# Kernel optimization log

Hardware: AMD Instinct MI355X
Metric: run time of the kernel (lower is better)

The kernel has to match this reference:

```python
import jax, jax.numpy as jnp
import numpy as np

G, N, F_IN, H, C = 128, 256, 128, 256, 10   # graphs, nodes/graph, in-feat, hidden, classes
NUM_NODES = G * N                            # 32768
E = NUM_NODES * 16                           # 524288 edges (avg degree 16)
K1, K2, K3 = 128, 64, 32                     # ceil(0.5*N) pooling chain per graph


def setup_inputs():
    key = jax.random.key(0)
    ks = jax.random.split(key, 16)
    def lin(k, fi, fo):
        return (jax.random.normal(k, (fi, fo), jnp.float32) / np.sqrt(fi).astype(np.float32))
    x = jax.random.normal(ks[0], (NUM_NODES, F_IN), jnp.float32)
    gid = jnp.repeat(jnp.arange(G), E // G)
    src = (gid * N + jax.random.randint(ks[1], (E,), 0, N)).astype(jnp.int32)
    dst = (gid * N + jax.random.randint(ks[2], (E,), 0, N)).astype(jnp.int32)
    edge_index = jnp.stack([src, dst])
    batch = jnp.repeat(jnp.arange(G), N).astype(jnp.int32)
    z32 = lambda *s: jnp.zeros(s, jnp.float32)
    return dict(
        x=x, edge_index=edge_index, batch=batch,
        conv1_W=lin(ks[3], F_IN, H), conv1_b=z32(H),
        conv2_W=lin(ks[4], H, H), conv2_b=z32(H),
        conv3_W=lin(ks[5], H, H), conv3_b=z32(H),
        pool1_rel_W=lin(ks[6], H, 1), pool1_rel_b=z32(1), pool1_root_W=lin(ks[7], H, 1),
        pool2_rel_W=lin(ks[8], H, 1), pool2_rel_b=z32(1), pool2_root_W=lin(ks[9], H, 1),
        fc1_W=lin(ks[10], 3 * H, H), fc1_b=z32(H),
        fc2_W=lin(ks[11], H, H // 2), fc2_b=z32(H // 2),
        fc3_W=lin(ks[12], H // 2, C), fc3_b=z32(C))


def _gcn(x, W, b, src, dst, emask, nmask):
    # PyG GCNConv: out = D^{-1/2}(A+I)D^{-1/2} (x W) + b, masked nodes/edges excluded.
    h = x @ W
    ew = emask.astype(x.dtype)
    deg = jax.ops.segment_sum(ew, dst, num_segments=NUM_NODES) + nmask  # +1 self-loop for active nodes
    dis = jnp.where(deg > 0, jax.lax.rsqrt(jnp.maximum(deg, 1e-12)), 0.0)
    norm = dis[src] * dis[dst] * ew
    out = jax.ops.segment_sum(h[src] * norm[:, None], dst, num_segments=NUM_NODES)
    out = out + h * (dis * dis * nmask)[:, None]  # self-loop message
    return out + b


def _sag_pool(x, src, dst, emask, nmask, k, w_rel, b_rel, w_root):
    # score = GraphConv(x): lin_root(x) + lin_rel(sum_j x_j); then top-k per graph, x *= tanh(score)
    ew = emask.astype(x.dtype)
    agg = jax.ops.segment_sum(x[src] * ew[:, None], dst, num_segments=NUM_NODES)
    score = (agg @ w_rel + b_rel + x @ w_root)[:, 0]
    score = jnp.where(nmask > 0, score, -jnp.inf)
    _, idx = jax.lax.top_k(score.reshape(G, N), k)           # [G, k] within-graph indices
    newmask = jnp.zeros((G, N), x.dtype).at[jnp.arange(G)[:, None], idx].set(1.0).reshape(-1)
    x = x * jnp.tanh(score)[:, None] * newmask[:, None]
    emask = emask & (newmask[src] > 0) & (newmask[dst] > 0)
    return x, emask, newmask


def _readout(x, nmask):
    xg = x.reshape(G, N, -1)
    m = nmask.reshape(G, N, 1)
    s = (xg * m).sum(axis=1)                                  # add-pool
    mean = s / m.sum(axis=1)                                  # mean-pool
    mx = jnp.max(jnp.where(m > 0, xg, -jnp.inf), axis=1)      # max-pool
    return jnp.concatenate([mean, mx, s], axis=-1)            # [G, 3H]


def reference(x, edge_index, batch, conv1_W, conv1_b, conv2_W, conv2_b, conv3_W, conv3_b,
              pool1_rel_W, pool1_rel_b, pool1_root_W, pool2_rel_W, pool2_rel_b, pool2_root_W,
              fc1_W, fc1_b, fc2_W, fc2_b, fc3_W, fc3_b):
    src, dst = edge_index[0], edge_index[1]
    nmask = jnp.ones((NUM_NODES,), x.dtype)
    emask = jnp.ones((E,), bool)
    h = jax.nn.relu(_gcn(x, conv1_W, conv1_b, src, dst, emask, nmask))
    h, emask, nmask = _sag_pool(h, src, dst, emask, nmask, K1, pool1_rel_W, pool1_rel_b, pool1_root_W)
    x1 = _readout(h, nmask)
    h = jax.nn.relu(_gcn(h, conv2_W, conv2_b, src, dst, emask, nmask))
    h, emask, nmask = _sag_pool(h, src, dst, emask, nmask, K2, pool2_rel_W, pool2_rel_b, pool2_root_W)
    x2 = _readout(h, nmask)
    h = jax.nn.relu(_gcn(h, conv3_W, conv3_b, src, dst, emask, nmask))
    # NB: original source reuses self.pool2 for the third pooling stage
    h, emask, nmask = _sag_pool(h, src, dst, emask, nmask, K3, pool2_rel_W, pool2_rel_b, pool2_root_W)
    x3 = _readout(h, nmask)
    z = x1 + x2 + x3
    z = jax.nn.relu(z @ fc1_W + fc1_b)
    z = jax.nn.relu(z @ fc2_W + fc2_b)          # dropout is identity in eval mode
    return jax.nn.log_softmax(z @ fc3_W + fc3_b, axis=-1)
```

## Files before the change

kernel.cpp:

```cpp
#include <hip/hip_runtime.h>
#include <math.h>

#define NG 128
#define NPG 256
#define NN 32768
#define HDIM 256
#define FIN 128

__global__ __launch_bounds__(256) void k_csr(const int* __restrict__ esrc,
                                             const int* __restrict__ edst, int EPG,
                                             int* __restrict__ rowptr, int* __restrict__ csr) {
    __shared__ int cnt[NPG];
    __shared__ int pref[NPG];
    __shared__ int cur[NPG];
    int g = blockIdx.x, tid = threadIdx.x;
    cnt[tid] = 0;
    __syncthreads();
    int base = g * EPG;
    for (int e = base + tid; e < base + EPG; e += 256)
        atomicAdd(&cnt[edst[e] & (NPG - 1)], 1);
    __syncthreads();
    int v = cnt[tid];
    pref[tid] = v;
    __syncthreads();
    for (int off = 1; off < NPG; off <<= 1) {
        int t = (tid >= off) ? pref[tid - off] : 0;
        __syncthreads();
        pref[tid] += t;
        __syncthreads();
    }
    int excl = pref[tid] - v;
    rowptr[g * NPG + tid] = base + excl;
    cur[tid] = base + excl;
    if (g == 0 && tid == 0) rowptr[NN] = NG * EPG;
    __syncthreads();
    for (int e = base + tid; e < base + EPG; e += 256) {
        int d = edst[e] & (NPG - 1);
        int p = atomicAdd(&cur[d], 1);
        csr[p] = esrc[e];
    }
}

__global__ __launch_bounds__(256) void k_sortw(const int* __restrict__ rowptr,
                                               int* __restrict__ csr,
                                               float* __restrict__ wedge) {
    int wid = (blockIdx.x * blockDim.x + threadIdx.x) >> 6;
    int lane = threadIdx.x & 63;
    if (wid >= NN) return;
    int e0 = rowptr[wid];
    int d = rowptr[wid + 1] - e0;
    if (d == 0) return;
    float ddst = rsqrtf((float)(1 + d));
    if (d <= 64) {
        int key = (lane < d) ? csr[e0 + lane] : 0x7fffffff;
        int rank = 0;
        for (int j = 0; j < d; j++) {
            int kj = __shfl(key, j);
            rank += (kj < key || (kj == key && j < lane)) ? 1 : 0;
        }
        if (lane < d) {
            csr[e0 + rank] = key;
            int sdeg = rowptr[key + 1] - rowptr[key];
            wedge[e0 + rank] = rsqrtf((float)(1 + sdeg)) * ddst;
        }
    } else if (lane == 0) {
        for (int a = e0 + 1; a < e0 + d; a++) {
            int key = csr[a];
            int b = a - 1;
            while (b >= e0 && csr[b] > key) { csr[b + 1] = csr[b]; b--; }
            csr[b + 1] = key;
        }
        for (int a = e0; a < e0 + d; a++) {
            int s = csr[a];
            wedge[a] = rsqrtf((float)(1 + rowptr[s + 1] - rowptr[s])) * ddst;
        }
    }
}

#define BM 64
#define BN 64
#define BK 16
#define BMP 68
__global__ __launch_bounds__(256) void k_sgemm(const float* __restrict__ A,
                                               const float* __restrict__ B,
                                               float* __restrict__ C, int K,
                                               const int* __restrict__ list,
                                               const float* __restrict__ brelu,
                                               const float* __restrict__ wrel,
                                               const float* __restrict__ wroot,
                                               float* __restrict__ rrel4,
                                               float* __restrict__ rroot4) {
    const int N = HDIM;
    __shared__ float As[BK][BMP];
    __shared__ float Bs[BK][BN];
    int tid = threadIdx.x;
    int tx = tid & 15, ty = tid >> 4;
    int row0 = blockIdx.y * BM, col0 = blockIdx.x * BN;
    int lm = tid >> 2;
    int arow = list ? list[row0 + lm] : (row0 + lm);
    int crow[4];
#pragma unroll
    for (int i = 0; i < 4; i++) {
        int r = row0 + ty * 4 + i;
        crow[i] = list ? list[r] : r;
    }
    float acc[4][4] = {};
    for (int kb = 0; kb < K; kb += BK) {
        {
            int k = (tid & 3) * 4;
            float4 av = *reinterpret_cast<const float4*>(&A[(size_t)arow * K + kb + k]);
            As[k + 0][lm] = av.x; As[k + 1][lm] = av.y; As[k + 2][lm] = av.z; As[k + 3][lm] = av.w;
        }
        {
            int l = tid * 4;
            int k = l >> 6, c = l & 63;
            *reinterpret_cast<float4*>(&Bs[k][c]) =
                *reinterpret_cast<const float4*>(&B[(size_t)(kb + k) * N + col0 + c]);
        }
        __syncthreads();
#pragma unroll
        for (int k = 0; k < BK; k++) {
            float4 a = *reinterpret_cast<float4*>(&As[k][ty * 4]);
            float4 b = *reinterpret_cast<float4*>(&Bs[k][tx * 4]);
            float av[4] = {a.x, a.y, a.z, a.w};
            float bv[4] = {b.x, b.y, b.z, b.w};
#pragma unroll
            for (int i = 0; i < 4; i++)
#pragma unroll
                for (int j = 0; j < 4; j++) acc[i][j] += av[i] * bv[j];
        }
        __syncthreads();
    }
    float4 bb = make_float4(0.f, 0.f, 0.f, 0.f);
    if (brelu) bb = *reinterpret_cast<const float4*>(&brelu[col0 + tx * 4]);
    float4 wr = make_float4(0.f, 0.f, 0.f, 0.f), wo = wr;
    if (wrel) {
        wr = *reinterpret_cast<const float4*>(&wrel[col0 + tx * 4]);
        wo = *reinterpret_cast<const float4*>(&wroot[col0 + tx * 4]);
    }
#pragma unroll
    for (int i = 0; i < 4; i++) {
        float4 v = make_float4(acc[i][0], acc[i][1], acc[i][2], acc[i][3]);
        if (brelu) {
            v.x = fmaxf(v.x + bb.x, 0.f);
            v.y = fmaxf(v.y + bb.y, 0.f);
            v.z = fmaxf(v.z + bb.z, 0.f);
            v.w = fmaxf(v.w + bb.w, 0.f);
        }
        *reinterpret_cast<float4*>(&C[(size_t)crow[i] * N + col0 + tx * 4]) = v;
        if (wrel) {
            float s1 = v.x * wr.x + v.y * wr.y + v.z * wr.z + v.w * wr.w;
            float s2 = v.x * wo.x + v.y * wo.y + v.z * wo.z + v.w * wo.w;
            for (int off = 8; off > 0; off >>= 1) {
                s1 += __shfl_down(s1, off, 16);
                s2 += __shfl_down(s2, off, 16);
            }
            if (tx == 0) {
                rrel4[(size_t)crow[i] * 4 + blockIdx.x] = s1;
                rroot4[(size_t)crow[i] * 4 + blockIdx.x] = s2;
            }
        }
    }
}

__device__ __forceinline__ int swz_block(int bid, int bpg) {
    int xcd = bid & 7, r = bid >> 3;
    int graph = xcd * (NG / 8) + r / bpg;
    int sub = r - (r / bpg) * bpg;
    return graph * bpg + sub;
}

__global__ __launch_bounds__(256) void k_aggx(const float* __restrict__ x,
                                              const int* __restrict__ rowptr,
                                              const int* __restrict__ csr,
                                              const float* __restrict__ wedge,
                                              float* __restrict__ xa) {
    int blk = swz_block(blockIdx.x, NPG / 8);
    int n = blk * 8 + (threadIdx.x >> 5);
    int lane = threadIdx.x & 31;
    const float4* xp = reinterpret_cast<const float4*>(x);
    int e0 = rowptr[n], e1 = rowptr[n + 1];
    float di = rsqrtf((float)(1 + e1 - e0));
    float4 h = xp[(size_t)n * (FIN / 4) + lane];
    float self = di * di;
    float ax = h.x * self, ay = h.y * self, az = h.z * self, aw = h.w * self;
    for (int e = e0; e < e1; e++) {
        int s = csr[e];
        float w = wedge[e];
        float4 hs = xp[(size_t)s * (FIN / 4) + lane];
        ax += hs.x * w; ay += hs.y * w; az += hs.z * w; aw += hs.w * w;
    }
    float4 o = make_float4(ax, ay, az, aw);
    reinterpret_cast<float4*>(xa)[(size_t)n * (FIN / 4) + lane] = o;
}

__global__ __launch_bounds__(256) void k_gcn_agg(const float* __restrict__ hW,
                                                 const float* __restrict__ dis,
                                                 const int* __restrict__ rowptr,
                                                 const int* __restrict__ csr,
                                                 const float* __restrict__ wedge,
                                                 const float* __restrict__ bias,
                                                 const int* __restrict__ list, int bpg,
                                                 const float* __restrict__ w_rel,
                                                 const float* __restrict__ w_root,
                                                 float* __restrict__ out,
                                                 float* __restrict__ r_rel,
                                                 float* __restrict__ r_root) {
    int blk = swz_block(blockIdx.x, bpg);
    int idx = blk * 4 + (threadIdx.x >> 6);
    int lane = threadIdx.x & 63;
    int wid = list[idx];
    float di = dis[wid];
    float4 h = *reinterpret_cast<const float4*>(&hW[(size_t)wid * HDIM + lane * 4]);
    float self = di * di;
    float ax = h.x * self, ay = h.y * self, az = h.z * self, aw = h.w * self;
    int e0 = rowptr[wid], e1 = rowptr[wid + 1];
    for (int e = e0; e < e1; e++) {
        float w = wedge[e];
        if (w > 0.f) {
            int s = csr[e];
            float4 hs = *reinterpret_cast<const float4*>(&hW[(size_t)s * HDIM + lane * 4]);
            ax += hs.x * w; ay += hs.y * w; az += hs.z * w; aw += hs.w * w;
        }
    }
    float4 b = *reinterpret_cast<const float4*>(&bias[lane * 4]);
    float4 o;
    o.x = fmaxf(ax + b.x, 0.f);
    o.y = fmaxf(ay + b.y, 0.f);
    o.z = fmaxf(az + b.z, 0.f);
    o.w = fmaxf(aw + b.w, 0.f);
    *reinterpret_cast<float4*>(&out[(size_t)wid * HDIM + lane * 4]) = o;
    float4 wr = *reinterpret_cast<const float4*>(&w_rel[lane * 4]);
    float4 wo = *reinterpret_cast<const float4*>(&w_root[lane * 4]);
    float s1 = o.x * wr.x + o.y * wr.y + o.z * wr.z + o.w * wr.w;
    float s2 = o.x * wo.x + o.y * wo.y + o.z * wo.z + o.w * wo.w;
    for (int off = 32; off > 0; off >>= 1) {
        s1 += __shfl_down(s1, off);
        s2 += __shfl_down(s2, off);
    }
    if (lane == 0) { r_rel[wid] = s1; r_root[wid] = s2; }
}

template<bool STAGE1, bool EMIT>
__global__ __launch_bounds__(256) void k_topkf(const float* __restrict__ dis,
                                               const int* __restrict__ rowptr,
                                               const int* __restrict__ csr,
                                               const float* __restrict__ r_rel,
                                               const float* __restrict__ r_root,
                                               const float* __restrict__ rrel4,
                                               const float* __restrict__ rroot4,
                                               const float* __restrict__ b_rel, int k,
                                               int* __restrict__ list,
                                               float* __restrict__ tansel,
                                               float* __restrict__ disN,
                                               float* __restrict__ wedgeN) {
    __shared__ float rrel[NPG];
    __shared__ float sc[NPG];
    __shared__ int pref[NPG];
    __shared__ int sels[NPG];
    __shared__ float disn[NPG];
    int g = blockIdx.x, tid = threadIdx.x;
    int n = g * NPG + tid;
    bool act = STAGE1 ? true : (dis[n] > 0.f);
    float rr, ro;
    if (STAGE1) {
        rr = ((rrel4[(size_t)n * 4 + 0] + rrel4[(size_t)n * 4 + 1]) +
              rrel4[(size_t)n * 4 + 2]) + rrel4[(size_t)n * 4 + 3];
        ro = ((rroot4[(size_t)n * 4 + 0] + rroot4[(size_t)n * 4 + 1]) +
              rroot4[(size_t)n * 4 + 2]) + rroot4[(size_t)n * 4 + 3];
    } else {
        rr = act ? r_rel[n] : 0.f;
        ro = act ? r_root[n] : 0.f;
    }
    rrel[tid] = act ? rr : 0.f;
    __syncthreads();
    int e0 = rowptr[n], e1 = rowptr[n + 1];
    float my;
    if (act) {
        float s = b_rel[0] + ro;
        for (int e = e0; e < e1; e++) s += rrel[csr[e] & (NPG - 1)];
        my = s;
    } else {
        my = -INFINITY;
    }
    sc[tid] = my;
    __syncthreads();
    int cnt = 0;
    for (int j = 0; j < NPG; j++) {
        float v = sc[j];
        cnt += (v > my || (v == my && j < tid)) ? 1 : 0;
    }
    int a = (cnt < k) ? 1 : 0;
    sels[tid] = a;
    pref[tid] = a;
    __syncthreads();
    for (int off = 1; off < NPG; off <<= 1) {
        int v = (tid >= off) ? pref[tid - off] : 0;
        __syncthreads();
        pref[tid] += v;
        __syncthreads();
    }
    if (a) {
        int rk = pref[tid] - 1;
        list[g * k + rk] = n;
        tansel[g * k + rk] = tanhf(my);
    }
    if (EMIT) {
        int c2 = 1;
        for (int e = e0; e < e1; e++) c2 += sels[csr[e] & (NPG - 1)];
        float dn = a ? rsqrtf((float)c2) : 0.f;
        disn[tid] = dn;
        disN[n] = dn;
        __syncthreads();
        if (a) {
            for (int e = e0; e < e1; e++) wedgeN[e] = disn[csr[e] & (NPG - 1)] * dn;
        }
    }
}

template<bool FIRST>
__global__ __launch_bounds__(256) void k_poolout2(float* __restrict__ h,
                                                  const float* __restrict__ tansel,
                                                  const int* __restrict__ list, int k,
                                                  float invk, float* __restrict__ z) {
    __shared__ float tv[128];
    __shared__ float red_s[4][64];
    __shared__ float red_m[4][64];
    int g = blockIdx.x >> 2, fc = blockIdx.x & 3;
    int tid = threadIdx.x;
    int x = tid & 63, y = tid >> 6;
    if (tid < k) tv[tid] = tansel[g * k + tid];
    __syncthreads();
    int f = fc * 64 + x;
    float s = 0.f, mx = -INFINITY;
    for (int idx = y; idx < k; idx += 4) {
        int node = list[g * k + idx];
        size_t p = (size_t)node * HDIM + f;
        float v = h[p] * tv[idx];
        h[p] = v;
        s += v;
        mx = fmaxf(mx, v);
    }
    red_s[y][x] = s;
    red_m[y][x] = mx;
    __syncthreads();
    if (y == 0) {
        s = red_s[0][x] + red_s[1][x] + red_s[2][x] + red_s[3][x];
        mx = fmaxf(fmaxf(red_m[0][x], red_m[1][x]), fmaxf(red_m[2][x], red_m[3][x]));
        if (FIRST) {
            z[g * 768 + f] = s * invk;
            z[g * 768 + 256 + f] = mx;
            z[g * 768 + 512 + f] = s;
        } else {
            z[g * 768 + f] += s * invk;
            z[g * 768 + 256 + f] += mx;
            z[g * 768 + 512 + f] += s;
        }
    }
}

__global__ __launch_bounds__(256) void k_fc1(const float* __restrict__ z,
                                             const float* __restrict__ W1,
                                             const float* __restrict__ b1,
                                             float* __restrict__ t1) {
    __shared__ float zb[768];
    __shared__ float red[4][64];
    int g = blockIdx.x >> 2, oc = blockIdx.x & 3;
    int tid = threadIdx.x;
    zb[tid] = z[g * 768 + tid];
    zb[tid + 256] = z[g * 768 + 256 + tid];
    zb[tid + 512] = z[g * 768 + 512 + tid];
    __syncthreads();
    int x = tid & 63, y = tid >> 6;
    int col = oc * 64 + x;
    float s = 0.f;
    for (int i = y * 192; i < (y + 1) * 192; i++) s += zb[i] * W1[(size_t)i * 256 + col];
    red[y][x] = s;
    __syncthreads();
    if (y == 0) {
        float t = red[0][x] + red[1][x] + red[2][x] + red[3][x] + b1[col];
        t1[g * 256 + col] = fmaxf(t, 0.f);
    }
}

__global__ __launch_bounds__(256) void k_fc2(const float* __restrict__ t1,
                                             const float* __restrict__ W2,
                                             const float* __restrict__ b2,
                                             float* __restrict__ t2) {
    __shared__ float t1s[256];
    __shared__ float red[4][64];
    int g = blockIdx.x >> 1, oc = blockIdx.x & 1;
    int tid = threadIdx.x;
    t1s[tid] = t1[g * 256 + tid];
    __syncthreads();
    int x = tid & 63, y = tid >> 6;
    int col = oc * 64 + x;
    float s = 0.f;
    for (int i = y * 64; i < (y + 1) * 64; i++) s += t1s[i] * W2[(size_t)i * 128 + col];
    red[y][x] = s;
    __syncthreads();
    if (y == 0) {
        float t = ((red[0][x] + red[1][x]) + red[2][x]) + red[3][x] + b2[col];
        t2[g * 128 + col] = fmaxf(t, 0.f);
    }
}

__global__ __launch_bounds__(256) void k_fc3(const float* __restrict__ t2,
                                             const float* __restrict__ W3,
                                             const float* __restrict__ b3,
                                             float* __restrict__ out) {
    __shared__ float t2s[128];
    __shared__ float t3[10];
    __shared__ float lse;
    int g = blockIdx.x, tid = threadIdx.x;
    if (tid < 128) t2s[tid] = t2[g * 128 + tid];
    __syncthreads();
    if (tid < 10) {
        float v = b3[tid];
        for (int i = 0; i < 128; i++) v += t2s[i] * W3[(size_t)i * 10 + tid];
        t3[tid] = v;
    }
    __syncthreads();
    if (tid == 0) {
        float m = t3[0];
        for (int c = 1; c < 10; c++) m = fmaxf(m, t3[c]);
        float se = 0.f;
        for (int c = 0; c < 10; c++) se += expf(t3[c] - m);
        lse = m + logf(se);
    }
    __syncthreads();
    if (tid < 10) out[g * 10 + tid] = t3[tid] - lse;
}

extern "C" void kernel_launch(void* const* d_in, const int* in_sizes, int n_in,
                              void* d_out, int out_size, void* d_ws, size_t ws_size,
                              hipStream_t stream) {
    const float* x        = (const float*)d_in[0];
    const int*   ei       = (const int*)d_in[1];
    const float* conv1_W  = (const float*)d_in[3];
    const float* conv1_b  = (const float*)d_in[4];
    const float* conv2_W  = (const float*)d_in[5];
    const float* conv2_b  = (const float*)d_in[6];
    const float* conv3_W  = (const float*)d_in[7];
    const float* conv3_b  = (const float*)d_in[8];
    const float* p1_relW  = (const float*)d_in[9];
    const float* p1_relb  = (const float*)d_in[10];
    const float* p1_rootW = (const float*)d_in[11];
    const float* p2_relW  = (const float*)d_in[12];
    const float* p2_relb  = (const float*)d_in[13];
    const float* p2_rootW = (const float*)d_in[14];
    const float* fc1_W    = (const float*)d_in[15];
    const float* fc1_b    = (const float*)d_in[16];
    const float* fc2_W    = (const float*)d_in[17];
    const float* fc2_b    = (const float*)d_in[18];
    const float* fc3_W    = (const float*)d_in[19];
    const float* fc3_b    = (const float*)d_in[20];
    float* out = (float*)d_out;

    const int E = in_sizes[1] / 2;
    const int EPG = E / NG;
    const int* e_src = ei;
    const int* e_dst = ei + E;

    char* base = (char*)d_ws;
    size_t off = 0;
    auto alloc = [&](size_t bytes) { size_t o = off; off = (off + bytes + 255) & ~(size_t)255; return o; };
    float* hW     = (float*)(base + alloc((size_t)NN * HDIM * 4));
    float* hcur   = (float*)(base + alloc((size_t)NN * HDIM * 4));
    float* dis    = (float*)(base + alloc(NN * 4));
    float* r_rel  = (float*)(base + alloc(NN * 4));
    float* r_root = (float*)(base + alloc(NN * 4));
    float* rrel4  = (float*)(base + alloc((size_t)NN * 4 * 4));
    float* rroot4 = (float*)(base + alloc((size_t)NN * 4 * 4));
    int*   rowptr = (int*)(base + alloc((NN + 1) * 4));
    int*   csr    = (int*)(base + alloc((size_t)E * 4));
    float* wedge  = (float*)(base + alloc((size_t)E * 4));
    float* z      = (float*)(base + alloc((size_t)NG * 768 * 4));
    float* t1buf  = (float*)(base + alloc((size_t)NG * 256 * 4));
    float* t2buf  = (float*)(base + alloc((size_t)NG * 128 * 4));
    int*   list1  = (int*)(base + alloc((size_t)NG * 128 * 4));
    int*   list2  = (int*)(base + alloc((size_t)NG * 64 * 4));
    int*   list3  = (int*)(base + alloc((size_t)NG * 32 * 4));
    float* tans1  = (float*)(base + alloc((size_t)NG * 128 * 4));
    float* tans2  = (float*)(base + alloc((size_t)NG * 64 * 4));
    float* tans3  = (float*)(base + alloc((size_t)NG * 32 * 4));

    k_csr<<<NG, 256, 0, stream>>>(e_src, e_dst, EPG, rowptr, csr);
    k_sortw<<<NN * 64 / 256, 256, 0, stream>>>(rowptr, csr, wedge);

    float* xa = hW;

    k_aggx<<<NN / 8, 256, 0, stream>>>(x, rowptr, csr, wedge, xa);
    {
        dim3 ggrid(HDIM / BN, NN / BM);
        k_sgemm<<<ggrid, 256, 0, stream>>>(xa, conv1_W, hcur, FIN, nullptr, conv1_b,
                                           p1_relW, p1_rootW, rrel4, rroot4);
    }
    k_topkf<true, true><<<NG, 256, 0, stream>>>(nullptr, rowptr, csr, nullptr, nullptr,
                                                rrel4, rroot4, p1_relb, 128,
                                                list1, tans1, dis, wedge);
    k_poolout2<true><<<NG * 4, 256, 0, stream>>>(hcur, tans1, list1, 128, 1.0f / 128.0f, z);

    {
        dim3 ggrid(HDIM / BN, (NG * 128) / BM);
        k_sgemm<<<ggrid, 256, 0, stream>>>(hcur, conv2_W, hW, HDIM, list1, nullptr,
                                           nullptr, nullptr, nullptr, nullptr);
    }
    k_gcn_agg<<<(NG * 128) / 4, 256, 0, stream>>>(hW, dis, rowptr, csr, wedge, conv2_b,
                                                  list1, 32, p2_relW, p2_rootW,
                                                  hcur, r_rel, r_root);
    k_topkf<false, true><<<NG, 256, 0, stream>>>(dis, rowptr, csr, r_rel, r_root,
                                                 nullptr, nullptr, p2_relb, 64,
                                                 list2, tans2, dis, wedge);
    k_poolout2<false><<<NG * 4, 256, 0, stream>>>(hcur, tans2, list2, 64, 1.0f / 64.0f, z);

    {
        dim3 ggrid(HDIM / BN, (NG * 64) / BM);
        k_sgemm<<<ggrid, 256, 0, stream>>>(hcur, conv3_W, hW, HDIM, list2, nullptr,
                                           nullptr, nullptr, nullptr, nullptr);
    }
    k_gcn_agg<<<(NG * 64) / 4, 256, 0, stream>>>(hW, dis, rowptr, csr, wedge, conv3_b,
                                                 list2, 16, p2_relW, p2_rootW,
                                                 hcur, r_rel, r_root);
    k_topkf<false, false><<<NG, 256, 0, stream>>>(dis, rowptr, csr, r_rel, r_root,
                                                  nullptr, nullptr, p2_relb, 32,
                                                  list3, tans3, nullptr, nullptr);
    k_poolout2<false><<<NG * 4, 256, 0, stream>>>(hcur, tans3, list3, 32, 1.0f / 32.0f, z);

    k_fc1<<<NG * 4, 256, 0, stream>>>(z, fc1_W, fc1_b, t1buf);
    k_fc2<<<NG * 2, 256, 0, stream>>>(t1buf, fc2_W, fc2_b, t2buf);
    k_fc3<<<NG, 256, 0, stream>>>(t2buf, fc3_W, fc3_b, out);
}
```

Before: 309.1 us.

## Fuse CSR sort with aggregation, top-k with pooling, and MLP layers; prefetch GEMM tiles

```diff
diff --git a/kernel.cpp b/kernel.cpp
--- a/kernel.cpp
+++ b/kernel.cpp
@@ -41,17 +41,27 @@
     }
 }
 
-__global__ __launch_bounds__(256) void k_sortw(const int* __restrict__ rowptr,
-                                               int* __restrict__ csr,
-                                               float* __restrict__ wedge) {
-    int wid = (blockIdx.x * blockDim.x + threadIdx.x) >> 6;
-    int lane = threadIdx.x & 63;
-    if (wid >= NN) return;
-    int e0 = rowptr[wid];
-    int d = rowptr[wid + 1] - e0;
-    if (d == 0) return;
+__device__ __forceinline__ int swz_block(int bid, int bpg) {
+    int xcd = bid & 7, r = bid >> 3;
+    int graph = xcd * (NG / 8) + r / bpg;
+    int sub = r - (r / bpg) * bpg;
+    return graph * bpg + sub;
+}
+
+__global__ __launch_bounds__(256) void k_sortagg(const float* __restrict__ x,
+                                                 const int* __restrict__ rowptr,
+                                                 int* __restrict__ csr,
+                                                 float* __restrict__ xa) {
+    __shared__ int skey[4][64];
+    __shared__ float swgt[4][64];
+    int blk = swz_block(blockIdx.x, NPG / 4);
+    int w = threadIdx.x >> 6, lane = threadIdx.x & 63;
+    int n = blk * 4 + w;
+    int e0 = rowptr[n];
+    int d = rowptr[n + 1] - e0;
     float ddst = rsqrtf((float)(1 + d));
-    if (d <= 64) {
+    bool big = d > 64;
+    if (!big) {
         int key = (lane < d) ? csr[e0 + lane] : 0x7fffffff;
         int rank = 0;
         for (int j = 0; j < d; j++) {
@@ -60,8 +70,8 @@
         }
         if (lane < d) {
             csr[e0 + rank] = key;
-            int sdeg = rowptr[key + 1] - rowptr[key];
-            wedge[e0 + rank] = rsqrtf((float)(1 + sdeg)) * ddst;
+            skey[w][rank] = key;
+            swgt[w][rank] = rsqrtf((float)(1 + rowptr[key + 1] - rowptr[key])) * ddst;
         }
     } else if (lane == 0) {
         for (int a = e0 + 1; a < e0 + d; a++) {
@@ -70,11 +80,30 @@
             while (b >= e0 && csr[b] > key) { csr[b + 1] = csr[b]; b--; }
             csr[b + 1] = key;
         }
-        for (int a = e0; a < e0 + d; a++) {
-            int s = csr[a];
-            wedge[a] = rsqrtf((float)(1 + rowptr[s + 1] - rowptr[s])) * ddst;
-        }
-    }
+    }
+    __syncthreads();
+    const float2* x2 = reinterpret_cast<const float2*>(x);
+    float di = ddst;
+    float2 h = x2[(size_t)n * (FIN / 2) + lane];
+    float self = di * di;
+    float ax = h.x * self, ay = h.y * self;
+    if (!big) {
+        for (int j = 0; j < d; j++) {
+            int s = skey[w][j];
+            float we = swgt[w][j];
+            float2 hs = x2[(size_t)s * (FIN / 2) + lane];
+            ax += hs.x * we; ay += hs.y * we;
+        }
+    } else {
+        for (int e = e0; e < e0 + d; e++) {
+            int s = csr[e];
+            float we = rsqrtf((float)(1 + rowptr[s + 1] - rowptr[s])) * ddst;
+            float2 hs = x2[(size_t)s * (FIN / 2) + lane];
+            ax += hs.x * we; ay += hs.y * we;
+        }
+    }
+    float2 o; o.x = ax; o.y = ay;
+    reinterpret_cast<float2*>(xa)[(size_t)n * (FIN / 2) + lane] = o;
 }
 
 #define BM 64
@@ -104,20 +133,20 @@
         int r = row0 + ty * 4 + i;
         crow[i] = list ? list[r] : r;
     }
+    int k4 = (tid & 3) * 4;
+    int kkB = tid >> 4, cB = (tid & 15) * 4;
+    float4 aP = *reinterpret_cast<const float4*>(&A[(size_t)arow * K + k4]);
+    float4 bP = *reinterpret_cast<const float4*>(&B[(size_t)kkB * N + col0 + cB]);
     float acc[4][4] = {};
     for (int kb = 0; kb < K; kb += BK) {
-        {
-            int k = (tid & 3) * 4;
-            float4 av = *reinterpret_cast<const float4*>(&A[(size_t)arow * K + kb + k]);
-            As[k + 0][lm] = av.x; As[k + 1][lm] = av.y; As[k + 2][lm] = av.z; As[k + 3][lm] = av.w;
-        }
-        {
-            int l = tid * 4;
-            int k = l >> 6, c = l & 63;
-            *reinterpret_cast<float4*>(&Bs[k][c]) =
-                *reinterpret_cast<const float4*>(&B[(size_t)(kb + k) * N + col0 + c]);
-        }
-        __syncthreads();
+        As[k4 + 0][lm] = aP.x; As[k4 + 1][lm] = aP.y;
+        As[k4 + 2][lm] = aP.z; As[k4 + 3][lm] = aP.w;
+        *reinterpret_cast<float4*>(&Bs[kkB][cB]) = bP;
+        __syncthreads();
+        if (kb + BK < K) {
+            aP = *reinterpret_cast<const float4*>(&A[(size_t)arow * K + kb + BK + k4]);
+            bP = *reinterpret_cast<const float4*>(&B[(size_t)(kb + BK + kkB) * N + col0 + cB]);
+        }
 #pragma unroll
         for (int k = 0; k < BK; k++) {
             float4 a = *reinterpret_cast<float4*>(&As[k][ty * 4]);
@@ -161,37 +190,6 @@
             }
         }
     }
-}
-
-__device__ __forceinline__ int swz_block(int bid, int bpg) {
-    int xcd = bid & 7, r = bid >> 3;
-    int graph = xcd * (NG / 8) + r / bpg;
-    int sub = r - (r / bpg) * bpg;
-    return graph * bpg + sub;
-}
-
-__global__ __launch_bounds__(256) void k_aggx(const float* __restrict__ x,
-                                              const int* __restrict__ rowptr,
-                                              const int* __restrict__ csr,
-                                              const float* __restrict__ wedge,
-                                              float* __restrict__ xa) {
-    int blk = swz_block(blockIdx.x, NPG / 8);
-    int n = blk * 8 + (threadIdx.x >> 5);
-    int lane = threadIdx.x & 31;
-    const float4* xp = reinterpret_cast<const float4*>(x);
-    int e0 = rowptr[n], e1 = rowptr[n + 1];
-    float di = rsqrtf((float)(1 + e1 - e0));
-    float4 h = xp[(size_t)n * (FIN / 4) + lane];
-    float self = di * di;
-    float ax = h.x * self, ay = h.y * self, az = h.z * self, aw = h.w * self;
-    for (int e = e0; e < e1; e++) {
-        int s = csr[e];
-        float w = wedge[e];
-        float4 hs = xp[(size_t)s * (FIN / 4) + lane];
-        ax += hs.x * w; ay += hs.y * w; az += hs.z * w; aw += hs.w * w;
-    }
-    float4 o = make_float4(ax, ay, az, aw);
-    reinterpret_cast<float4*>(xa)[(size_t)n * (FIN / 4) + lane] = o;
 }
 
 __global__ __launch_bounds__(256) void k_gcn_agg(const float* __restrict__ hW,
@@ -241,25 +239,31 @@
     if (lane == 0) { r_rel[wid] = s1; r_root[wid] = s2; }
 }
 
-template<bool STAGE1, bool EMIT>
-__global__ __launch_bounds__(256) void k_topkf(const float* __restrict__ dis,
-                                               const int* __restrict__ rowptr,
-                                               const int* __restrict__ csr,
-                                               const float* __restrict__ r_rel,
-                                               const float* __restrict__ r_root,
-                                               const float* __restrict__ rrel4,
-                                               const float* __restrict__ rroot4,
-                                               const float* __restrict__ b_rel, int k,
-                                               int* __restrict__ list,
-                                               float* __restrict__ tansel,
-                                               float* __restrict__ disN,
-                                               float* __restrict__ wedgeN) {
+template<bool STAGE1, bool EMIT, bool FIRST>
+__global__ __launch_bounds__(256) void k_topkpool(const float* __restrict__ dis,
+                                                  const int* __restrict__ rowptr,
+                                                  const int* __restrict__ csr,
+                                                  const float* __restrict__ r_rel,
+                                                  const float* __restrict__ r_root,
+                                                  const float* __restrict__ rrel4,
+                                                  const float* __restrict__ rroot4,
+                                                  const float* __restrict__ b_rel, int k,
+                                                  int* __restrict__ list,
+                                                  float* __restrict__ h,
+                                                  float* __restrict__ z, float invk,
+                                                  float* __restrict__ disN,
+                                                  float* __restrict__ wedgeN) {
     __shared__ float rrel[NPG];
     __shared__ float sc[NPG];
     __shared__ int pref[NPG];
     __shared__ int sels[NPG];
     __shared__ float disn[NPG];
-    int g = blockIdx.x, tid = threadIdx.x;
+    __shared__ int newl[128];
+    __shared__ float tvsel[128];
+    __shared__ float red_s[4][64];
+    __shared__ float red_m[4][64];
+    int g = blockIdx.x >> 2, fc = blockIdx.x & 3;
+    int tid = threadIdx.x;
     int n = g * NPG + tid;
     bool act = STAGE1 ? true : (dis[n] > 0.f);
     float rr, ro;
@@ -302,51 +306,39 @@
     }
     if (a) {
         int rk = pref[tid] - 1;
-        list[g * k + rk] = n;
-        tansel[g * k + rk] = tanhf(my);
+        newl[rk] = tid;
+        tvsel[rk] = tanhf(my);
+        if (fc == 0 && list) list[g * k + rk] = n;
     }
     if (EMIT) {
         int c2 = 1;
         for (int e = e0; e < e1; e++) c2 += sels[csr[e] & (NPG - 1)];
         float dn = a ? rsqrtf((float)c2) : 0.f;
         disn[tid] = dn;
-        disN[n] = dn;
-        __syncthreads();
-        if (a) {
+        if (fc == 0) disN[n] = dn;
+        __syncthreads();
+        if (a && fc == 0) {
             for (int e = e0; e < e1; e++) wedgeN[e] = disn[csr[e] & (NPG - 1)] * dn;
         }
     }
-}
-
-template<bool FIRST>
-__global__ __launch_bounds__(256) void k_poolout2(float* __restrict__ h,
-                                                  const float* __restrict__ tansel,
-                                                  const int* __restrict__ list, int k,
-                                                  float invk, float* __restrict__ z) {
-    __shared__ float tv[128];
-    __shared__ float red_s[4][64];
-    __shared__ float red_m[4][64];
-    int g = blockIdx.x >> 2, fc = blockIdx.x & 3;
-    int tid = threadIdx.x;
-    int x = tid & 63, y = tid >> 6;
-    if (tid < k) tv[tid] = tansel[g * k + tid];
-    __syncthreads();
-    int f = fc * 64 + x;
+    __syncthreads();
+    int xq = tid & 63, y = tid >> 6;
+    int f = fc * 64 + xq;
     float s = 0.f, mx = -INFINITY;
     for (int idx = y; idx < k; idx += 4) {
-        int node = list[g * k + idx];
+        int node = g * NPG + newl[idx];
         size_t p = (size_t)node * HDIM + f;
-        float v = h[p] * tv[idx];
+        float v = h[p] * tvsel[idx];
         h[p] = v;
         s += v;
         mx = fmaxf(mx, v);
     }
-    red_s[y][x] = s;
-    red_m[y][x] = mx;
+    red_s[y][xq] = s;
+    red_m[y][xq] = mx;
     __syncthreads();
     if (y == 0) {
-        s = red_s[0][x] + red_s[1][x] + red_s[2][x] + red_s[3][x];
-        mx = fmaxf(fmaxf(red_m[0][x], red_m[1][x]), fmaxf(red_m[2][x], red_m[3][x]));
+        s = red_s[0][xq] + red_s[1][xq] + red_s[2][xq] + red_s[3][xq];
+        mx = fmaxf(fmaxf(red_m[0][xq], red_m[1][xq]), fmaxf(red_m[2][xq], red_m[3][xq]));
         if (FIRST) {
             z[g * 768 + f] = s * invk;
             z[g * 768 + 256 + f] = mx;
@@ -359,65 +351,44 @@
     }
 }
 
-__global__ __launch_bounds__(256) void k_fc1(const float* __restrict__ z,
-                                             const float* __restrict__ W1,
-                                             const float* __restrict__ b1,
-                                             float* __restrict__ t1) {
+__global__ __launch_bounds__(256) void k_mlp(const float* __restrict__ z,
+                                             const float* __restrict__ W1, const float* __restrict__ b1,
+                                             const float* __restrict__ W2, const float* __restrict__ b2,
+                                             const float* __restrict__ W3, const float* __restrict__ b3,
+                                             float* __restrict__ out) {
     __shared__ float zb[768];
-    __shared__ float red[4][64];
-    int g = blockIdx.x >> 2, oc = blockIdx.x & 3;
-    int tid = threadIdx.x;
+    __shared__ float t1[256];
+    __shared__ float t2[128];
+    __shared__ float t3[10];
+    __shared__ float lse;
+    int g = blockIdx.x, tid = threadIdx.x;
     zb[tid] = z[g * 768 + tid];
     zb[tid + 256] = z[g * 768 + 256 + tid];
     zb[tid + 512] = z[g * 768 + 512 + tid];
     __syncthreads();
-    int x = tid & 63, y = tid >> 6;
-    int col = oc * 64 + x;
-    float s = 0.f;
-    for (int i = y * 192; i < (y + 1) * 192; i++) s += zb[i] * W1[(size_t)i * 256 + col];
-    red[y][x] = s;
-    __syncthreads();
-    if (y == 0) {
-        float t = red[0][x] + red[1][x] + red[2][x] + red[3][x] + b1[col];
-        t1[g * 256 + col] = fmaxf(t, 0.f);
-    }
-}
-
-__global__ __launch_bounds__(256) void k_fc2(const float* __restrict__ t1,
-                                             const float* __restrict__ W2,
-                                             const float* __restrict__ b2,
-                                             float* __restrict__ t2) {
-    __shared__ float t1s[256];
-    __shared__ float red[4][64];
-    int g = blockIdx.x >> 1, oc = blockIdx.x & 1;
-    int tid = threadIdx.x;
-    t1s[tid] = t1[g * 256 + tid];
-    __syncthreads();
-    int x = tid & 63, y = tid >> 6;
-    int col = oc * 64 + x;
-    float s = 0.f;
-    for (int i = y * 64; i < (y + 1) * 64; i++) s += t1s[i] * W2[(size_t)i * 128 + col];
-    red[y][x] = s;
-    __syncthreads();
-    if (y == 0) {
-        float t = ((red[0][x] + red[1][x]) + red[2][x]) + red[3][x] + b2[col];
-        t2[g * 128 + col] = fmaxf(t, 0.f);
-    }
-}
-
-__global__ __launch_bounds__(256) void k_fc3(const float* __restrict__ t2,
-                                             const float* __restrict__ W3,
-                                             const float* __restrict__ b3,
-                                             float* __restrict__ out) {
-    __shared__ float t2s[128];
-    __shared__ float t3[10];
-    __shared__ float lse;
-    int g = blockIdx.x, tid = threadIdx.x;
-    if (tid < 128) t2s[tid] = t2[g * 128 + tid];
+    {
+        int col = tid;
+        float r0 = 0.f, r1 = 0.f, r2 = 0.f, r3 = 0.f;
+        for (int i = 0;   i < 192; i++) r0 += zb[i] * W1[(size_t)i * 256 + col];
+        for (int i = 192; i < 384; i++) r1 += zb[i] * W1[(size_t)i * 256 + col];
+        for (int i = 384; i < 576; i++) r2 += zb[i] * W1[(size_t)i * 256 + col];
+        for (int i = 576; i < 768; i++) r3 += zb[i] * W1[(size_t)i * 256 + col];
+        t1[col] = fmaxf(r0 + r1 + r2 + r3 + b1[col], 0.f);
+    }
+    __syncthreads();
+    if (tid < 128) {
+        int col = tid;
+        float r0 = 0.f, r1 = 0.f, r2 = 0.f, r3 = 0.f;
+        for (int i = 0;   i < 64;  i++) r0 += t1[i] * W2[(size_t)i * 128 + col];
+        for (int i = 64;  i < 128; i++) r1 += t1[i] * W2[(size_t)i * 128 + col];
+        for (int i = 128; i < 192; i++) r2 += t1[i] * W2[(size_t)i * 128 + col];
+        for (int i = 192; i < 256; i++) r3 += t1[i] * W2[(size_t)i * 128 + col];
+        t2[col] = fmaxf(((r0 + r1) + r2) + r3 + b2[col], 0.f);
+    }
     __syncthreads();
     if (tid < 10) {
         float v = b3[tid];
-        for (int i = 0; i < 128; i++) v += t2s[i] * W3[(size_t)i * 10 + tid];
+        for (int i = 0; i < 128; i++) v += t2[i] * W3[(size_t)i * 10 + tid];
         t3[tid] = v;
     }
     __syncthreads();
@@ -468,6 +439,7 @@
     float* hW     = (float*)(base + alloc((size_t)NN * HDIM * 4));
     float* hcur   = (float*)(base + alloc((size_t)NN * HDIM * 4));
     float* dis    = (float*)(base + alloc(NN * 4));
+    float* dis2   = (float*)(base + alloc(NN * 4));
     float* r_rel  = (float*)(base + alloc(NN * 4));
     float* r_root = (float*)(base + alloc(NN * 4));
     float* rrel4  = (float*)(base + alloc((size_t)NN * 4 * 4));
@@ -476,30 +448,21 @@
     int*   csr    = (int*)(base + alloc((size_t)E * 4));
     float* wedge  = (float*)(base + alloc((size_t)E * 4));
     float* z      = (float*)(base + alloc((size_t)NG * 768 * 4));
-    float* t1buf  = (float*)(base + alloc((size_t)NG * 256 * 4));
-    float* t2buf  = (float*)(base + alloc((size_t)NG * 128 * 4));
     int*   list1  = (int*)(base + alloc((size_t)NG * 128 * 4));
     int*   list2  = (int*)(base + alloc((size_t)NG * 64 * 4));
-    int*   list3  = (int*)(base + alloc((size_t)NG * 32 * 4));
-    float* tans1  = (float*)(base + alloc((size_t)NG * 128 * 4));
-    float* tans2  = (float*)(base + alloc((size_t)NG * 64 * 4));
-    float* tans3  = (float*)(base + alloc((size_t)NG * 32 * 4));
 
     k_csr<<<NG, 256, 0, stream>>>(e_src, e_dst, EPG, rowptr, csr);
-    k_sortw<<<NN * 64 / 256, 256, 0, stream>>>(rowptr, csr, wedge);
-
     float* xa = hW;
-
-    k_aggx<<<NN / 8, 256, 0, stream>>>(x, rowptr, csr, wedge, xa);
+    k_sortagg<<<NN / 4, 256, 0, stream>>>(x, rowptr, csr, xa);
+
     {
         dim3 ggrid(HDIM / BN, NN / BM);
         k_sgemm<<<ggrid, 256, 0, stream>>>(xa, conv1_W, hcur, FIN, nullptr, conv1_b,
                                            p1_relW, p1_rootW, rrel4, rroot4);
     }
-    k_topkf<true, true><<<NG, 256, 0, stream>>>(nullptr, rowptr, csr, nullptr, nullptr,
-                                                rrel4, rroot4, p1_relb, 128,
-                                                list1, tans1, dis, wedge);
-    k_poolout2<true><<<NG * 4, 256, 0, stream>>>(hcur, tans1, list1, 128, 1.0f / 128.0f, z);
+    k_topkpool<true, true, true><<<NG * 4, 256, 0, stream>>>(
+        nullptr, rowptr, csr, nullptr, nullptr, rrel4, rroot4, p1_relb, 128,
+        list1, hcur, z, 1.0f / 128.0f, dis, wedge);
 
     {
         dim3 ggrid(HDIM / BN, (NG * 128) / BM);
@@ -509,25 +472,21 @@
     k_gcn_agg<<<(NG * 128) / 4, 256, 0, stream>>>(hW, dis, rowptr, csr, wedge, conv2_b,
                                                   list1, 32, p2_relW, p2_rootW,
                                                   hcur, r_rel, r_root);
-    k_topkf<false, true><<<NG, 256, 0, stream>>>(dis, rowptr, csr, r_rel, r_root,
-                                                 nullptr, nullptr, p2_relb, 64,
-                                                 list2, tans2, dis, wedge);
-    k_poolout2<false><<<NG * 4, 256, 0, stream>>>(hcur, tans2, list2, 64, 1.0f / 64.0f, z);
+    k_topkpool<false, true, false><<<NG * 4, 256, 0, stream>>>(
+        dis, rowptr, csr, r_rel, r_root, nullptr, nullptr, p2_relb, 64,
+        list2, hcur, z, 1.0f / 64.0f, dis2, wedge);
 
     {
         dim3 ggrid(HDIM / BN, (NG * 64) / BM);
         k_sgemm<<<ggrid, 256, 0, stream>>>(hcur, conv3_W, hW, HDIM, list2, nullptr,
                                            nullptr, nullptr, nullptr, nullptr);
     }
-    k_gcn_agg<<<(NG * 64) / 4, 256, 0, stream>>>(hW, dis, rowptr, csr, wedge, conv3_b,
+    k_gcn_agg<<<(NG * 64) / 4, 256, 0, stream>>>(hW, dis2, rowptr, csr, wedge, conv3_b,
                                                  list2, 16, p2_relW, p2_rootW,
                                                  hcur, r_rel, r_root);
-    k_topkf<false, false><<<NG, 256, 0, stream>>>(dis, rowptr, csr, r_rel, r_root,
-                                                  nullptr, nullptr, p2_relb, 32,
-                                                  list3, tans3, nullptr, nullptr);
-    k_poolout2<false><<<NG * 4, 256, 0, stream>>>(hcur, tans3, list3, 32, 1.0f / 32.0f, z);
-
-    k_fc1<<<NG * 4, 256, 0, stream>>>(z, fc1_W, fc1_b, t1buf);
-    k_fc2<<<NG * 2, 256, 0, stream>>>(t1buf, fc2_W, fc2_b, t2buf);
-    k_fc3<<<NG, 256, 0, stream>>>(t2buf, fc3_W, fc3_b, out);
-}
+    k_topkpool<false, false, false><<<NG * 4, 256, 0, stream>>>(
+        dis2, rowptr, csr, r_rel, r_root, nullptr, nullptr, p2_relb, 32,
+        nullptr, hcur, z, 1.0f / 32.0f, nullptr, nullptr);
+
+    k_mlp<<<NG, 256, 0, stream>>>(z, fc1_W, fc1_b, fc2_W, fc2_b, fc3_W, fc3_b, out);
+}
```

Result: faster. 294.1 us (-4.8%).
